# Kernel optimization log

Hardware: AMD Instinct MI355X
Metric: run time of the kernel (lower is better)

## Reference

```python
import jax, jax.numpy as jnp
import numpy as np

N = 128   # n_features == out_dim (required by the Christoffel permutes)
H = 256   # MLP hidden width of forward_func
B = 16    # batch size (state_batch is [2B, N])
EPS_G = 1e-4
EPS_DG = 1e-6
EPS_V = 1e-6


def setup_inputs() -> dict:
    key = jax.random.key(0)
    ks = jax.random.split(key, 6)
    return {
        "t": jax.random.uniform(ks[0], (), dtype=jnp.float32),
        "state_batch": jax.random.normal(ks[1], (2 * B, N), dtype=jnp.float32) * 0.1,
        "x0_batch": jax.random.normal(ks[2], (B, N), dtype=jnp.float32),
        "x1_batch": jax.random.normal(ks[3], (B, N), dtype=jnp.float32),
        "W1": jax.random.normal(ks[4], (N, H), dtype=jnp.float32) / np.float32(np.sqrt(N)),
        "b1": jnp.zeros((H,), dtype=jnp.float32),
        "W2": jax.random.normal(ks[5], (H, N), dtype=jnp.float32) / np.float32(np.sqrt(H)),
        "b2": jnp.zeros((N,), dtype=jnp.float32),
    }


def reference(t, state_batch, x0_batch, x1_batch, W1, b1, W2, b2):
    def f(x):  # forward_func, per-sample: [N] -> [N]
        return jnp.tanh(x @ W1 + b1) @ W2 + b2

    def metric(x):  # G(x) = J J^T + 1e-4 I, per-sample: [N] -> [N, N]
        J = jax.jacrev(f)(x)                      # [N, N], matches per-output grad loop
        return J @ J.T + EPS_G * jnp.eye(N, dtype=x.dtype)

    deviation, dev_velocity = jnp.split(state_batch, 2, axis=0)  # each [B, N]
    window = 4.0 * t * (1.0 - t)
    # x along the perturbed straight path
    x = x0_batch + t * (x1_batch - x0_batch) + window * deviation  # [B, N]

    # dG[b, i, j, k] = dG_ij/dx_k -- replaces the out_dim^2 autograd.grad loop
    dG = jax.vmap(jax.jacfwd(metric))(x)  # [B, N, N, N]
    nrm = jnp.sqrt(jnp.sum(dG * dG, axis=(1, 2, 3), keepdims=True))
    dG = dG / (nrm + EPS_DG)

    # Christoffel-like symbols
    Gamma = 0.5 * (dG + jnp.transpose(dG, (0, 2, 1, 3)) - jnp.transpose(dG, (0, 3, 1, 2)))
    a = -jnp.einsum('bijk,bj,bk->bi', Gamma, dev_velocity, dev_velocity)
    a = a / (jnp.linalg.norm(dev_velocity, axis=1, keepdims=True) + EPS_V)

    restoration = -0.1 * deviation
    return jnp.concatenate([dev_velocity, a + restoration], axis=0)  # [2B, N]
```

## Files before the change

### kernel.cpp

```cpp
#include <hip/hip_runtime.h>
#include <math.h>


static constexpr int OFF_W2T  = 0;
static constexpr int OFF_S    = 32768;
static constexpr int OFF_Q    = 98304;
static constexpr int OFF_D    = 163840;
static constexpr int OFF_C    = 167936;
static constexpr int OFF_UV   = 172032;
static constexpr int OFF_AV   = 176128;
static constexpr int OFF_VN   = 180224;
static constexpr int OFF_SUM  = 180240;
static constexpr int OFF_CNT  = 180256;
static constexpr int OFF_PT   = 180272;
static constexpr int OFF_PN   = OFF_PT + 16 * 32768;

__global__ __launch_bounds__(256) void k_stage1(const float* __restrict__ tptr,
                                                const float* __restrict__ state,
                                                const float* __restrict__ x0,
                                                const float* __restrict__ x1,
                                                const float* __restrict__ W1,
                                                const float* __restrict__ b1,
                                                const float* __restrict__ W2,
                                                float* __restrict__ ws,
                                                float* __restrict__ out) {
    __shared__ __align__(16) float smem[2 * 32 * 34];
    int blk = blockIdx.x;
    int tid = threadIdx.x;

    if (blk < 64) {
        float* Ai = smem;
        float* Aj = smem + 1088;
        int m0 = (blk >> 3) * 32, n0 = (blk & 7) * 32;
        int lx = tid & 31, lr = tid >> 5;
        int tx = tid & 15, ty = tid >> 4;
        float a00 = 0, a01 = 0, a10 = 0, a11 = 0;
        for (int kc = 0; kc < 128; kc += 32) {
            #pragma unroll
            for (int i = 0; i < 4; ++i) {
                int k = lr + 8 * i;
                Ai[k * 34 + lx] = W1[(kc + k) * 256 + m0 + lx];
                Aj[k * 34 + lx] = W1[(kc + k) * 256 + n0 + lx];
            }
            __syncthreads();
            #pragma unroll
            for (int k = 0; k < 32; ++k) {
                float2 a = *(const float2*)&Ai[k * 34 + 2 * ty];
                float2 b = *(const float2*)&Aj[k * 34 + 2 * tx];
                a00 += a.x * b.x; a01 += a.x * b.y;
                a10 += a.y * b.x; a11 += a.y * b.y;
            }
            __syncthreads();
        }
        float* S = ws + OFF_S;
        int m = m0 + 2 * ty, n = n0 + 2 * tx;
        S[m * 256 + n]           = a00;
        S[m * 256 + n + 1]       = a01;
        S[(m + 1) * 256 + n]     = a10;
        S[(m + 1) * 256 + n + 1] = a11;
    } else if (blk < 128) {
        float* Xi = smem;
        float* Xj = smem + 1088;
        int bq = blk - 64;
        int m0 = (bq >> 3) * 32, n0 = (bq & 7) * 32;
        int lx = tid & 31, lr = tid >> 5;
        int tx = tid & 15, ty = tid >> 4;
        float a00 = 0, a01 = 0, a10 = 0, a11 = 0;
        for (int kc = 0; kc < 128; kc += 32) {
            #pragma unroll
            for (int i = 0; i < 4; ++i) {
                Xi[lx * 34 + lr + 8 * i] = W2[(m0 + lr + 8 * i) * 128 + kc + lx];
                Xj[lx * 34 + lr + 8 * i] = W2[(n0 + lr + 8 * i) * 128 + kc + lx];
            }
            __syncthreads();
            #pragma unroll
            for (int k = 0; k < 32; ++k) {
                float2 a = *(const float2*)&Xi[k * 34 + 2 * ty];
                float2 b = *(const float2*)&Xj[k * 34 + 2 * tx];
                a00 += a.x * b.x; a01 += a.x * b.y;
                a10 += a.y * b.x; a11 += a.y * b.y;
            }
            __syncthreads();
        }
        float* Q = ws + OFF_Q;
        int m = m0 + 2 * ty, n = n0 + 2 * tx;
        Q[m * 256 + n]           = a00;
        Q[m * 256 + n + 1]       = a01;
        Q[(m + 1) * 256 + n]     = a10;
        Q[(m + 1) * 256 + n + 1] = a11;
    } else if (blk < 160) {
        float* tile = smem;
        int b2 = blk - 128;
        int c0 = (b2 & 3) * 32, r0 = (b2 >> 2) * 32;
        int tx = tid & 31, ty = tid >> 5;
        #pragma unroll
        for (int i = 0; i < 32; i += 8)
            tile[(ty + i) * 33 + tx] = W2[(r0 + ty + i) * 128 + c0 + tx];
        __syncthreads();
        float* W2T = ws + OFF_W2T;
        #pragma unroll
        for (int i = 0; i < 32; i += 8)
            W2T[(c0 + ty + i) * 256 + r0 + tx] = tile[tx * 33 + ty + i];
    } else {
        int b = blk - 160;
        float* xs  = smem;
        float* vs  = smem + 128;
        float* red = smem + 256;
        float t = tptr[0];
        float w = 4.f * t * (1.f - t);
        if (tid == 0) {
            ws[OFF_SUM + b] = 0.f;
            ((int*)(ws + OFF_CNT))[b] = 0;
        }
        if (tid < 128) {
            float dev = state[b * 128 + tid];
            float v   = state[(16 + b) * 128 + tid];
            float xv  = x0[b * 128 + tid] + t * (x1[b * 128 + tid] - x0[b * 128 + tid]) + w * dev;
            xs[tid] = xv;
            vs[tid] = v;
            out[b * 128 + tid] = v;
            red[tid] = v * v;
        }
        __syncthreads();
        for (int s = 64; s > 0; s >>= 1) {
            if (tid < s) red[tid] += red[tid + s];
            __syncthreads();
        }
        if (tid == 0) ws[OFF_VN + b] = sqrtf(red[0]);

        int m = tid;
        float h = b1[m], uvm = 0.f;
        #pragma unroll 8
        for (int k = 0; k < 128; ++k) {
            float wv = W1[k * 256 + m];
            h   += xs[k] * wv;
            uvm += vs[k] * wv;
        }
        float z  = tanhf(h);
        float dd = 1.f - z * z;
        float cc = -2.f * z * dd;
        const float4* w2r = (const float4*)&W2[m * 128];
        const float4* vs4 = (const float4*)vs;
        float avm = 0.f;
        #pragma unroll 8
        for (int j4 = 0; j4 < 32; ++j4) {
            float4 ww = w2r[j4];
            float4 vv = vs4[j4];
            avm += ww.x * vv.x + ww.y * vv.y + ww.z * vv.z + ww.w * vv.w;
        }
        ws[OFF_D  + b * 256 + m] = dd;
        ws[OFF_C  + b * 256 + m] = cc;
        ws[OFF_UV + b * 256 + m] = uvm;
        ws[OFF_AV + b * 256 + m] = avm;
    }
}

__global__ __launch_bounds__(256) void k_pmat3(const float* __restrict__ Smat,
                                               const float* __restrict__ dall,
                                               const float* __restrict__ W2,
                                               float* __restrict__ PT,
                                               float* __restrict__ Pn) {
    __shared__ __align__(16) float ST[32 * 36];
    __shared__ __align__(16) float YT[32 * 68];
    int b = blockIdx.z, mt = blockIdx.y, jt = blockIdx.x;
    int m0 = mt * 32, j0 = jt * 64;
    const float* dvec = dall + b * 256;
    int tid = threadIdx.x;
    int n = tid >> 3, c4 = (tid & 7) * 4;
    int ty = tid >> 5, tx = tid & 31;
    float acc[4][2] = {};
    for (int nc = 0; nc < 256; nc += 32) {
        *(float4*)&ST[n * 36 + c4] = *(const float4*)&Smat[(nc + n) * 256 + m0 + c4];
        float dn = dvec[nc + n];
        #pragma unroll
        for (int i = 0; i < 2; ++i) {
            int col = c4 + 32 * i;
            float4 wv = *(const float4*)&W2[(nc + n) * 128 + j0 + col];
            wv.x *= dn; wv.y *= dn; wv.z *= dn; wv.w *= dn;
            *(float4*)&YT[n * 68 + col] = wv;
        }
        __syncthreads();
        #pragma unroll 8
        for (int k = 0; k < 32; ++k) {
            float4 a  = *(const float4*)&ST[k * 36 + 4 * ty];
            float2 bb = *(const float2*)&YT[k * 68 + 2 * tx];
            acc[0][0] += a.x * bb.x; acc[0][1] += a.x * bb.y;
            acc[1][0] += a.y * bb.x; acc[1][1] += a.y * bb.y;
            acc[2][0] += a.z * bb.x; acc[2][1] += a.z * bb.y;
            acc[3][0] += a.w * bb.x; acc[3][1] += a.w * bb.y;
        }
        __syncthreads();
    }
    float* ptb = PT + b * 32768;
    float* pnb = Pn + b * 32768;
    #pragma unroll
    for (int jj = 0; jj < 2; ++jj) {
        float4 v = make_float4(acc[0][jj], acc[1][jj], acc[2][jj], acc[3][jj]);
        *(float4*)&ptb[(j0 + 2 * tx + jj) * 256 + m0 + 4 * ty] = v;
    }
    #pragma unroll
    for (int ii = 0; ii < 4; ++ii) {
        float2 v = make_float2(acc[ii][0], acc[ii][1]);
        *(float2*)&pnb[(m0 + 4 * ty + ii) * 128 + j0 + 2 * tx] = v;
    }
}

__global__ __launch_bounds__(256, 3) void k_fnorm6(const float* __restrict__ state,
                                                   const float* __restrict__ W2,
                                                   float* __restrict__ ws,
                                                   float* __restrict__ out) {
    __shared__ __align__(16) float lds[12544];
    int blk = blockIdx.x;
    int tid = threadIdx.x;
    int* cnt = (int*)(ws + OFF_CNT);

    if (blk < 16) {
        int b = blk;
        const float* ptb = ws + OFF_PT + b * 32768;
        const float* pnb = ws + OFF_PN + b * 32768;
        float* vs   = lds;
        float* g1   = lds + 128;
        float* g2   = lds + 384;
        float* red  = lds + 640;
        float* snrm = lds + 900;
        if (tid < 128) vs[tid] = state[(16 + b) * 128 + tid];
        __syncthreads();

        int m = tid;
        float pv = 0.f;
        #pragma unroll 8
        for (int j = 0; j < 128; ++j)
            pv += ptb[j * 256 + m] * vs[j];
        float cc  = ws[OFF_C  + b * 256 + m];
        float uvm = ws[OFF_UV + b * 256 + m];
        float avm = ws[OFF_AV + b * 256 + m];
        g1[m] = cc * pv  * uvm;
        g2[m] = cc * avm * uvm;
        __syncthreads();

        int i = tid & 127, half = tid >> 7;
        int mmlo = half * 128;
        float raw = 0.f;
        #pragma unroll 8
        for (int mm = mmlo; mm < mmlo + 128; ++mm)
            raw += W2[mm * 128 + i] * g1[mm] + pnb[mm * 128 + i] * g2[mm];
        red[tid] = raw;
        __syncthreads();

        if (tid == 0) {
            while (atomicAdd(&cnt[b], 0) < 36) __builtin_amdgcn_s_sleep(2);
            __threadfence();
            float tot = atomicAdd(&ws[OFF_SUM + b], 0.0f);
            snrm[0] = sqrtf(fmaxf(2.f * tot, 0.f));
        }
        __syncthreads();
        if (tid < 128) {
            float rawt = red[tid] + red[tid + 128];
            float vn = ws[OFF_VN + b];
            float a  = -0.5f * rawt / ((snrm[0] + 1e-6f) * (vn + 1e-6f));
            out[(16 + b) * 128 + tid] = a - 0.1f * state[b * 128 + tid];
        }
        return;
    }

    int q   = blk - 16;
    int idx = q >> 4;
    int b   = q & 15;
    int tj = 0;
    while ((tj + 1) * (tj + 2) / 2 <= idx) ++tj;
    int ti = idx - tj * (tj + 1) / 2;
    int mi0 = ti * 32, mj0 = tj * 32;
    float* PiT = lds;
    float* PjT = lds + 2048;
    float* WiT = lds + 4096;
    float* WjT = lds + 6144;
    const float* ptb = ws + OFF_PT + b * 32768;
    const float* W2T = ws + OFF_W2T;
    const float* Smat = ws + OFF_S;
    const float* Qmat = ws + OFF_Q;
    int jr = tid >> 3, jc4 = (tid & 7) * 4;
    int w = tid >> 6, s = tid & 63;
    int ty = s >> 3, tx = s & 7;
    float r[4][4] = {}, f[4][4] = {}, g[4][4] = {};
    #pragma unroll
    for (int rr = 0; rr < 2; ++rr) {
        #pragma unroll
        for (int it = 0; it < 2; ++it) {
            int l = jr + 32 * it;
            int j = 32 * (l >> 4) + 16 * rr + (l & 15);
            *(float4*)&PiT[l * 32 + jc4] = *(const float4*)&ptb[j * 256 + mi0 + jc4];
            *(float4*)&PjT[l * 32 + jc4] = *(const float4*)&ptb[j * 256 + mj0 + jc4];
            *(float4*)&WiT[l * 32 + jc4] = *(const float4*)&W2T[j * 256 + mi0 + jc4];
            *(float4*)&WjT[l * 32 + jc4] = *(const float4*)&W2T[j * 256 + mj0 + jc4];
        }
        __syncthreads();
        #pragma unroll 4
        for (int jj = 0; jj < 16; ++jj) {
            int l = 16 * w + jj;
            float4 pi4 = *(const float4*)&PiT[l * 32 + 4 * ty];
            float4 pj4 = *(const float4*)&PjT[l * 32 + 4 * tx];
            float4 wi4 = *(const float4*)&WiT[l * 32 + 4 * ty];
            float4 wj4 = *(const float4*)&WjT[l * 32 + 4 * tx];
            float pi[4] = {pi4.x, pi4.y, pi4.z, pi4.w};
            float pj[4] = {pj4.x, pj4.y, pj4.z, pj4.w};
            float wi[4] = {wi4.x, wi4.y, wi4.z, wi4.w};
            float wj[4] = {wj4.x, wj4.y, wj4.z, wj4.w};
            #pragma unroll
            for (int ii = 0; ii < 4; ++ii)
                #pragma unroll
                for (int kk = 0; kk < 4; ++kk) {
                    r[ii][kk] += pi[ii] * pj[kk];
                    f[ii][kk] += pi[ii] * wj[kk];
                    g[ii][kk] += pj[kk] * wi[ii];
                }
        }
        __syncthreads();
    }
    {
        float* scr = lds;
        int base = tid * 49;
        #pragma unroll
        for (int ii = 0; ii < 4; ++ii)
            #pragma unroll
            for (int kk = 0; kk < 4; ++kk) {
                scr[base + ii * 4 + kk]      = r[ii][kk];
                scr[base + 16 + ii * 4 + kk] = f[ii][kk];
                scr[base + 32 + ii * 4 + kk] = g[ii][kk];
            }
    }
    __syncthreads();
    if (tid < 64) {
        const float* scr = lds;
        float tr[16], tf[16], tg[16];
        #pragma unroll
        for (int k = 0; k < 16; ++k) {
            tr[k] = scr[tid * 49 + k]           + scr[(tid + 64) * 49 + k]
                  + scr[(tid + 128) * 49 + k]   + scr[(tid + 192) * 49 + k];
            tf[k] = scr[tid * 49 + 16 + k]      + scr[(tid + 64) * 49 + 16 + k]
                  + scr[(tid + 128) * 49 + 16 + k] + scr[(tid + 192) * 49 + 16 + k];
            tg[k] = scr[tid * 49 + 32 + k]      + scr[(tid + 64) * 49 + 32 + k]
                  + scr[(tid + 128) * 49 + 32 + k] + scr[(tid + 192) * 49 + 32 + k];
        }
        const float* cb = ws + OFF_C + b * 256;
        int mi = mi0 + 4 * (tid >> 3), mj = mj0 + 4 * (tid & 7);
        float4 ce4 = *(const float4*)&cb[mj];
        float ce[4] = {ce4.x, ce4.y, ce4.z, ce4.w};
        float sum = 0.f;
        #pragma unroll
        for (int ii = 0; ii < 4; ++ii) {
            float ci = cb[mi + ii];
            float4 S4 = *(const float4*)&Smat[(mi + ii) * 256 + mj];
            float4 Q4 = *(const float4*)&Qmat[(mi + ii) * 256 + mj];
            float Sv[4] = {S4.x, S4.y, S4.z, S4.w};
            float Qv[4] = {Q4.x, Q4.y, Q4.z, Q4.w};
            #pragma unroll
            for (int kk = 0; kk < 4; ++kk)
                sum += ci * ce[kk] * Sv[kk] * (Qv[kk] * tr[ii * 4 + kk] + tf[ii * 4 + kk] * tg[ii * 4 + kk]);
        }
        if (ti < tj) sum *= 2.f;
        #pragma unroll
        for (int off = 32; off > 0; off >>= 1)
            sum += __shfl_down(sum, off);
        if (tid == 0) {
            atomicAdd(&ws[OFF_SUM + b], sum);
            __threadfence();
            atomicAdd(&cnt[b], 1);
        }
    }
}

extern "C" void kernel_launch(void* const* d_in, const int* in_sizes, int n_in,
                              void* d_out, int out_size, void* d_ws, size_t ws_size,
                              hipStream_t stream) {
    (void)in_sizes; (void)n_in; (void)out_size; (void)ws_size;
    const float* t     = (const float*)d_in[0];
    const float* state = (const float*)d_in[1];
    const float* x0    = (const float*)d_in[2];
    const float* x1    = (const float*)d_in[3];
    const float* W1    = (const float*)d_in[4];
    const float* b1    = (const float*)d_in[5];
    const float* W2    = (const float*)d_in[6];
    float* out = (float*)d_out;
    float* ws  = (float*)d_ws;

    k_stage1<<<176, 256, 0, stream>>>(t, state, x0, x1, W1, b1, W2, ws, out);
    k_pmat3<<<dim3(2, 8, 16), 256, 0, stream>>>(ws + OFF_S, ws + OFF_D, W2,
                                                ws + OFF_PT, ws + OFF_PN);
    k_fnorm6<<<592, 256, 0, stream>>>(state, W2, ws, out);
}
```

Baseline: 115.0 us.

## Fuse P-matrix computation into stage1 kernel, recomputing from W1 to drop a launch

Removes the separate k_pmat3 launch. The 128 extra blocks in the first kernel compute P directly as W1·(W1ᵀ·diag(d)·W2), recomputing the hidden activations per block, instead of reading the precomputed S matrix from stage 1. The Q-Gram and W2-transpose blocks are packed two tiles per block to make room. This trades one kernel launch and the dependency on S for redundant tanh/hidden recomputation and more FLOPs per batch element (W1ᵀY then W1F). The PT offset is also realigned.

```diff
diff --git a/kernel.cpp b/kernel.cpp
--- a/kernel.cpp
+++ b/kernel.cpp
@@ -12,25 +12,25 @@
 static constexpr int OFF_VN   = 180224;
 static constexpr int OFF_SUM  = 180240;
 static constexpr int OFF_CNT  = 180256;
-static constexpr int OFF_PT   = 180272;
+static constexpr int OFF_PT   = 180288;
 static constexpr int OFF_PN   = OFF_PT + 16 * 32768;
 
-__global__ __launch_bounds__(256) void k_stage1(const float* __restrict__ tptr,
-                                                const float* __restrict__ state,
-                                                const float* __restrict__ x0,
-                                                const float* __restrict__ x1,
-                                                const float* __restrict__ W1,
-                                                const float* __restrict__ b1,
-                                                const float* __restrict__ W2,
-                                                float* __restrict__ ws,
-                                                float* __restrict__ out) {
-    __shared__ __align__(16) float smem[2 * 32 * 34];
+__global__ __launch_bounds__(256) void k_stage1b(const float* __restrict__ tptr,
+                                                 const float* __restrict__ state,
+                                                 const float* __restrict__ x0,
+                                                 const float* __restrict__ x1,
+                                                 const float* __restrict__ W1,
+                                                 const float* __restrict__ b1,
+                                                 const float* __restrict__ W2,
+                                                 float* __restrict__ ws,
+                                                 float* __restrict__ out) {
+    __shared__ __align__(16) float lds[8192];
     int blk = blockIdx.x;
     int tid = threadIdx.x;
 
     if (blk < 64) {
-        float* Ai = smem;
-        float* Aj = smem + 1088;
+        float* Ai = lds;
+        float* Aj = lds + 1088;
         int m0 = (blk >> 3) * 32, n0 = (blk & 7) * 32;
         int lx = tid & 31, lr = tid >> 5;
         int tx = tid & 15, ty = tid >> 4;
@@ -58,59 +58,67 @@
         S[m * 256 + n + 1]       = a01;
         S[(m + 1) * 256 + n]     = a10;
         S[(m + 1) * 256 + n + 1] = a11;
+    } else if (blk < 96) {
+        int bqq = blk - 64;
+        for (int hh = 0; hh < 2; ++hh) {
+            int bq = bqq + 32 * hh;
+            float* Xi = lds;
+            float* Xj = lds + 1088;
+            int m0 = (bq >> 3) * 32, n0 = (bq & 7) * 32;
+            int lx = tid & 31, lr = tid >> 5;
+            int tx = tid & 15, ty = tid >> 4;
+            float a00 = 0, a01 = 0, a10 = 0, a11 = 0;
+            for (int kc = 0; kc < 128; kc += 32) {
+                #pragma unroll
+                for (int i = 0; i < 4; ++i) {
+                    Xi[lx * 34 + lr + 8 * i] = W2[(m0 + lr + 8 * i) * 128 + kc + lx];
+                    Xj[lx * 34 + lr + 8 * i] = W2[(n0 + lr + 8 * i) * 128 + kc + lx];
+                }
+                __syncthreads();
+                #pragma unroll
+                for (int k = 0; k < 32; ++k) {
+                    float2 a = *(const float2*)&Xi[k * 34 + 2 * ty];
+                    float2 b = *(const float2*)&Xj[k * 34 + 2 * tx];
+                    a00 += a.x * b.x; a01 += a.x * b.y;
+                    a10 += a.y * b.x; a11 += a.y * b.y;
+                }
+                __syncthreads();
+            }
+            float* Q = ws + OFF_Q;
+            int m = m0 + 2 * ty, n = n0 + 2 * tx;
+            Q[m * 256 + n]           = a00;
+            Q[m * 256 + n + 1]       = a01;
+            Q[(m + 1) * 256 + n]     = a10;
+            Q[(m + 1) * 256 + n + 1] = a11;
+            __syncthreads();
+        }
+    } else if (blk < 112) {
+        int bt = blk - 96;
+        for (int hh = 0; hh < 2; ++hh) {
+            int b2 = bt + 16 * hh;
+            float* tile = lds;
+            int c0 = (b2 & 3) * 32, r0 = (b2 >> 2) * 32;
+            int tx = tid & 31, ty = tid >> 5;
+            #pragma unroll
+            for (int i = 0; i < 32; i += 8)
+                tile[(ty + i) * 33 + tx] = W2[(r0 + ty + i) * 128 + c0 + tx];
+            __syncthreads();
+            float* W2T = ws + OFF_W2T;
+            #pragma unroll
+            for (int i = 0; i < 32; i += 8)
+                W2T[(c0 + ty + i) * 256 + r0 + tx] = tile[tx * 33 + ty + i];
+            __syncthreads();
+        }
     } else if (blk < 128) {
-        float* Xi = smem;
-        float* Xj = smem + 1088;
-        int bq = blk - 64;
-        int m0 = (bq >> 3) * 32, n0 = (bq & 7) * 32;
-        int lx = tid & 31, lr = tid >> 5;
-        int tx = tid & 15, ty = tid >> 4;
-        float a00 = 0, a01 = 0, a10 = 0, a11 = 0;
-        for (int kc = 0; kc < 128; kc += 32) {
-            #pragma unroll
-            for (int i = 0; i < 4; ++i) {
-                Xi[lx * 34 + lr + 8 * i] = W2[(m0 + lr + 8 * i) * 128 + kc + lx];
-                Xj[lx * 34 + lr + 8 * i] = W2[(n0 + lr + 8 * i) * 128 + kc + lx];
-            }
-            __syncthreads();
-            #pragma unroll
-            for (int k = 0; k < 32; ++k) {
-                float2 a = *(const float2*)&Xi[k * 34 + 2 * ty];
-                float2 b = *(const float2*)&Xj[k * 34 + 2 * tx];
-                a00 += a.x * b.x; a01 += a.x * b.y;
-                a10 += a.y * b.x; a11 += a.y * b.y;
-            }
-            __syncthreads();
-        }
-        float* Q = ws + OFF_Q;
-        int m = m0 + 2 * ty, n = n0 + 2 * tx;
-        Q[m * 256 + n]           = a00;
-        Q[m * 256 + n + 1]       = a01;
-        Q[(m + 1) * 256 + n]     = a10;
-        Q[(m + 1) * 256 + n + 1] = a11;
-    } else if (blk < 160) {
-        float* tile = smem;
-        int b2 = blk - 128;
-        int c0 = (b2 & 3) * 32, r0 = (b2 >> 2) * 32;
-        int tx = tid & 31, ty = tid >> 5;
-        #pragma unroll
-        for (int i = 0; i < 32; i += 8)
-            tile[(ty + i) * 33 + tx] = W2[(r0 + ty + i) * 128 + c0 + tx];
-        __syncthreads();
-        float* W2T = ws + OFF_W2T;
-        #pragma unroll
-        for (int i = 0; i < 32; i += 8)
-            W2T[(c0 + ty + i) * 256 + r0 + tx] = tile[tx * 33 + ty + i];
-    } else {
-        int b = blk - 160;
-        float* xs  = smem;
-        float* vs  = smem + 128;
-        float* red = smem + 256;
+        int b = blk - 112;
+        float* xs  = lds;
+        float* vs  = lds + 128;
+        float* red = lds + 256;
         float t = tptr[0];
         float w = 4.f * t * (1.f - t);
         if (tid == 0) {
             ws[OFF_SUM + b] = 0.f;
-            ((int*)(ws + OFF_CNT))[b] = 0;
+            ((int*)ws)[OFF_CNT + b] = 0;
         }
         if (tid < 128) {
             float dev = state[b * 128 + tid];
@@ -152,56 +160,93 @@
         ws[OFF_C  + b * 256 + m] = cc;
         ws[OFF_UV + b * 256 + m] = uvm;
         ws[OFF_AV + b * 256 + m] = avm;
-    }
-}
-
-__global__ __launch_bounds__(256) void k_pmat3(const float* __restrict__ Smat,
-                                               const float* __restrict__ dall,
-                                               const float* __restrict__ W2,
-                                               float* __restrict__ PT,
-                                               float* __restrict__ Pn) {
-    __shared__ __align__(16) float ST[32 * 36];
-    __shared__ __align__(16) float YT[32 * 68];
-    int b = blockIdx.z, mt = blockIdx.y, jt = blockIdx.x;
-    int m0 = mt * 32, j0 = jt * 64;
-    const float* dvec = dall + b * 256;
-    int tid = threadIdx.x;
-    int n = tid >> 3, c4 = (tid & 7) * 4;
-    int ty = tid >> 5, tx = tid & 31;
-    float acc[4][2] = {};
-    for (int nc = 0; nc < 256; nc += 32) {
-        *(float4*)&ST[n * 36 + c4] = *(const float4*)&Smat[(nc + n) * 256 + m0 + c4];
-        float dn = dvec[nc + n];
-        #pragma unroll
-        for (int i = 0; i < 2; ++i) {
-            int col = c4 + 32 * i;
-            float4 wv = *(const float4*)&W2[(nc + n) * 128 + j0 + col];
-            wv.x *= dn; wv.y *= dn; wv.z *= dn; wv.w *= dn;
-            *(float4*)&YT[n * 68 + col] = wv;
-        }
-        __syncthreads();
-        #pragma unroll 8
-        for (int k = 0; k < 32; ++k) {
-            float4 a  = *(const float4*)&ST[k * 36 + 4 * ty];
-            float2 bb = *(const float2*)&YT[k * 68 + 2 * tx];
-            acc[0][0] += a.x * bb.x; acc[0][1] += a.x * bb.y;
-            acc[1][0] += a.y * bb.x; acc[1][1] += a.y * bb.y;
-            acc[2][0] += a.z * bb.x; acc[2][1] += a.z * bb.y;
-            acc[3][0] += a.w * bb.x; acc[3][1] += a.w * bb.y;
-        }
-        __syncthreads();
-    }
-    float* ptb = PT + b * 32768;
-    float* pnb = Pn + b * 32768;
-    #pragma unroll
-    for (int jj = 0; jj < 2; ++jj) {
-        float4 v = make_float4(acc[0][jj], acc[1][jj], acc[2][jj], acc[3][jj]);
-        *(float4*)&ptb[(j0 + 2 * tx + jj) * 256 + m0 + 4 * ty] = v;
-    }
-    #pragma unroll
-    for (int ii = 0; ii < 4; ++ii) {
-        float2 v = make_float2(acc[ii][0], acc[ii][1]);
-        *(float2*)&pnb[(m0 + 4 * ty + ii) * 128 + j0 + 2 * tx] = v;
+    } else {
+        int q = blk - 128;
+        int b = q >> 3, jt = q & 7, j0 = jt * 16;
+        float* xs  = lds;
+        float* dsv = lds + 128;
+        float* W1s = lds + 384;
+        float* YdT = lds + 4992;
+        float* Fl  = lds + 5568;
+        float t = tptr[0];
+        float w = 4.f * t * (1.f - t);
+        if (tid < 128) {
+            float dev = state[b * 128 + tid];
+            xs[tid] = x0[b * 128 + tid] + t * (x1[b * 128 + tid] - x0[b * 128 + tid]) + w * dev;
+        }
+        __syncthreads();
+        {
+            int m = tid;
+            float h = b1[m];
+            #pragma unroll 8
+            for (int k = 0; k < 128; ++k) h += xs[k] * W1[k * 256 + m];
+            float z = tanhf(h);
+            dsv[m] = 1.f - z * z;
+        }
+        __syncthreads();
+
+        float facc[8] = {};
+        int pj = tid & 15, pk = tid >> 4;
+        for (int nc = 0; nc < 256; nc += 32) {
+            {
+                int r = tid >> 1, h16 = (tid & 1) * 16;
+                #pragma unroll
+                for (int c = 0; c < 4; ++c)
+                    *(float4*)&W1s[r * 36 + h16 + 4 * c] =
+                        *(const float4*)&W1[r * 256 + nc + h16 + 4 * c];
+            }
+            if (tid < 128) {
+                int n2 = tid >> 2, c4 = (tid & 3) * 4;
+                float4 wv = *(const float4*)&W2[(nc + n2) * 128 + j0 + c4];
+                float dn = dsv[nc + n2];
+                YdT[(c4 + 0) * 36 + n2] = wv.x * dn;
+                YdT[(c4 + 1) * 36 + n2] = wv.y * dn;
+                YdT[(c4 + 2) * 36 + n2] = wv.z * dn;
+                YdT[(c4 + 3) * 36 + n2] = wv.w * dn;
+            }
+            __syncthreads();
+            #pragma unroll
+            for (int nn = 0; nn < 32; nn += 4) {
+                float4 yv = *(const float4*)&YdT[pj * 36 + nn];
+                #pragma unroll
+                for (int kk = 0; kk < 8; ++kk) {
+                    float4 wv = *(const float4*)&W1s[(pk + 16 * kk) * 36 + nn];
+                    facc[kk] += wv.x * yv.x; facc[kk] += wv.y * yv.y;
+                    facc[kk] += wv.z * yv.z; facc[kk] += wv.w * yv.w;
+                }
+            }
+            __syncthreads();
+        }
+        #pragma unroll
+        for (int kk = 0; kk < 8; ++kk)
+            Fl[(pk + 16 * kk) * 20 + pj] = facc[kk];
+        __syncthreads();
+
+        float acc2[16] = {};
+        int m = tid;
+        #pragma unroll 4
+        for (int k = 0; k < 128; ++k) {
+            float wv = W1[k * 256 + m];
+            const float4* fr = (const float4*)&Fl[k * 20];
+            float4 f0 = fr[0], f1 = fr[1], f2 = fr[2], f3 = fr[3];
+            acc2[0]  += wv * f0.x; acc2[1]  += wv * f0.y;
+            acc2[2]  += wv * f0.z; acc2[3]  += wv * f0.w;
+            acc2[4]  += wv * f1.x; acc2[5]  += wv * f1.y;
+            acc2[6]  += wv * f1.z; acc2[7]  += wv * f1.w;
+            acc2[8]  += wv * f2.x; acc2[9]  += wv * f2.y;
+            acc2[10] += wv * f2.z; acc2[11] += wv * f2.w;
+            acc2[12] += wv * f3.x; acc2[13] += wv * f3.y;
+            acc2[14] += wv * f3.z; acc2[15] += wv * f3.w;
+        }
+        float* ptb = ws + OFF_PT + b * 32768;
+        float* pnb = ws + OFF_PN + b * 32768;
+        #pragma unroll
+        for (int jj = 0; jj < 16; ++jj)
+            ptb[(j0 + jj) * 256 + m] = acc2[jj];
+        #pragma unroll
+        for (int q4 = 0; q4 < 4; ++q4)
+            *(float4*)&pnb[m * 128 + j0 + 4 * q4] =
+                make_float4(acc2[4 * q4], acc2[4 * q4 + 1], acc2[4 * q4 + 2], acc2[4 * q4 + 3]);
     }
 }
 
@@ -212,7 +257,7 @@
     __shared__ __align__(16) float lds[12544];
     int blk = blockIdx.x;
     int tid = threadIdx.x;
-    int* cnt = (int*)(ws + OFF_CNT);
+    int* cnt = (int*)ws + OFF_CNT;
 
     if (blk < 16) {
         int b = blk;
@@ -274,8 +319,8 @@
     float* PjT = lds + 2048;
     float* WiT = lds + 4096;
     float* WjT = lds + 6144;
-    const float* ptb = ws + OFF_PT + b * 32768;
-    const float* W2T = ws + OFF_W2T;
+    const float* ptb  = ws + OFF_PT + b * 32768;
+    const float* W2T  = ws + OFF_W2T;
     const float* Smat = ws + OFF_S;
     const float* Qmat = ws + OFF_Q;
     int jr = tid >> 3, jc4 = (tid & 7) * 4;
@@ -383,8 +428,6 @@
     float* out = (float*)d_out;
     float* ws  = (float*)d_ws;
 
-    k_stage1<<<176, 256, 0, stream>>>(t, state, x0, x1, W1, b1, W2, ws, out);
-    k_pmat3<<<dim3(2, 8, 16), 256, 0, stream>>>(ws + OFF_S, ws + OFF_D, W2,
-                                                ws + OFF_PT, ws + OFF_PN);
+    k_stage1b<<<256, 256, 0, stream>>>(t, state, x0, x1, W1, b1, W2, ws, out);
     k_fnorm6<<<592, 256, 0, stream>>>(state, W2, ws, out);
 }
```

New measurement: 118.6 us. +3.1%, slower.
